# Optimization experiments

Hardware: AMD Instinct MI355X
Metric: run time of the kernel (lower is better)

Reference implementation:

```python
import jax, jax.numpy as jnp
import numpy as np

N_NODES = 50000
N_EDGES = 800000
IN_CH, HID_CH, OUT_CH = 128, 256, 128
BN_EPS = 1e-5


def gcn_conv(x, W, b, src, dst):
    """PyG GCNConv: h = x @ W; symmetric normalization with self-loops; scatter-add; + bias."""
    N = x.shape[0]
    h = x @ W  # [N, out_ch]
    # degree including self-loop (all edge weights = 1)
    deg = jax.ops.segment_sum(jnp.ones(src.shape[0], h.dtype), dst, num_segments=N) + 1.0
    dis = jax.lax.rsqrt(deg)  # deg^-1/2
    norm = dis[src] * dis[dst]  # [E]
    agg = jax.ops.segment_sum(h[src] * norm[:, None], dst, num_segments=N)
    # self-loop contribution: norm_ii = dis[i]^2
    return agg + h * (dis * dis)[:, None] + b


def batchnorm_train(x, gamma, beta):
    mu = jnp.mean(x, axis=0)
    var = jnp.mean((x - mu) ** 2, axis=0)  # biased var, as torch BN uses for normalization
    return (x - mu) * jax.lax.rsqrt(var + BN_EPS) * gamma + beta


def setup_inputs() -> dict:
    key = jax.random.key(0)
    ks = jax.random.split(key, 4)
    x = jax.random.normal(ks[0], (N_NODES, IN_CH), dtype=jnp.float32)
    edge_index = jax.random.randint(ks[1], (2, N_EDGES), 0, N_NODES, dtype=jnp.int64 if jax.config.jax_enable_x64 else jnp.int32)
    W1 = jax.random.normal(ks[2], (IN_CH, HID_CH), dtype=jnp.float32) * (1.0 / np.sqrt(IN_CH))
    W2 = jax.random.normal(ks[3], (HID_CH, OUT_CH), dtype=jnp.float32) * (1.0 / np.sqrt(HID_CH))
    return {
        "x": x,
        "edge_index": edge_index,
        "W1": W1,
        "b1": jnp.zeros((HID_CH,), jnp.float32),
        "gamma1": jnp.ones((HID_CH,), jnp.float32),
        "beta1": jnp.zeros((HID_CH,), jnp.float32),
        "W2": W2,
        "b2": jnp.zeros((OUT_CH,), jnp.float32),
    }


def reference(x, edge_index, W1, b1, gamma1, beta1, W2, b2):
    src, dst = edge_index[0], edge_index[1]
    h = gcn_conv(x, W1, b1, src, dst)
    h = jax.nn.relu(batchnorm_train(h, gamma1, beta1))
    # dropout omitted (deterministic eval-style reference)
    return gcn_conv(h, W2, b2, src, dst)
```

## Files before the change

kernel.cpp:

```cpp
#include <hip/hip_runtime.h>

#define N_NODES 50000
#define N_EDGES 800000
#define C_IN 128
#define C_HID 256
#define C_OUT 128
#define BN_EPS 1e-5f

typedef __bf16 v8bf __attribute__((ext_vector_type(8)));
typedef float f32x4 __attribute__((ext_vector_type(4)));

static __device__ __forceinline__ unsigned short f2bf(float f) {
    unsigned int u = __float_as_uint(f);
    u += 0x7fffu + ((u >> 16) & 1u);
    return (unsigned short)(u >> 16);
}
static __device__ __forceinline__ float bf2f(unsigned short h) {
    return __uint_as_float((unsigned int)h << 16);
}
static __device__ __forceinline__ unsigned int pack2(float a, float b) {
    return (unsigned int)f2bf(a) | ((unsigned int)f2bf(b) << 16);
}
static __device__ __forceinline__ float lo2f(unsigned int u) { return __uint_as_float(u << 16); }
static __device__ __forceinline__ float hi2f(unsigned int u) { return __uint_as_float(u & 0xffff0000u); }

#define DEG_BLOCKS ((N_EDGES + 255) / 256)


__global__ __launch_bounds__(256) void k_deg_wtrans(const int* __restrict__ dst, int* __restrict__ deg,
                                                    const float* __restrict__ W1, const float* __restrict__ W2,
                                                    unsigned short* __restrict__ WT1, unsigned short* __restrict__ WT2) {
    int bx = blockIdx.x, t = threadIdx.x;
    if (bx < DEG_BLOCKS) {
        int e = bx * 256 + t;
        if (e < N_EDGES) atomicAdd(&deg[dst[e]], 1);
    } else {
        int i = (bx - DEG_BLOCKS) * 256 + t;
        if (i < C_IN * C_HID) {
            int n = i >> 7, k = i & 127;
            WT1[n * C_IN + k] = f2bf(W1[k * C_HID + n]);
        } else {
            int j = i - C_IN * C_HID;
            int n = j >> 8, k = j & 255;
            WT2[n * C_HID + k] = f2bf(W2[k * C_OUT + n]);
        }
    }
}


__global__ __launch_bounds__(512) void k_scan1(const int* __restrict__ deg, int* __restrict__ rs,
                                               int* __restrict__ partial, float* __restrict__ dis) {
    __shared__ int s[512];
    int t = threadIdx.x;
    int i = blockIdx.x * 512 + t;
    int v = (i < N_NODES) ? deg[i] : 0;
    if (i < N_NODES) dis[i] = rsqrtf((float)v + 1.0f);
    s[t] = v;
    __syncthreads();
    for (int off = 1; off < 512; off <<= 1) {
        int tv = (t >= off) ? s[t - off] : 0;
        __syncthreads();
        s[t] += tv;
        __syncthreads();
    }
    if (i < N_NODES) rs[i + 1] = s[t];
    if (t == 511) partial[blockIdx.x] = s[511];
}

__global__ __launch_bounds__(256) void k_scan23(int* __restrict__ rs, const int* __restrict__ partial,
                                                int* __restrict__ cur, int nb) {
    __shared__ int pre[128];
    __shared__ int wsum[2];
    int t = threadIdx.x;
    int lane = t & 63;
    int pv = 0, v = 0;
    if (t < 128) {
        pv = (t < nb) ? partial[t] : 0;
        v = pv;
#pragma unroll
        for (int off = 1; off < 64; off <<= 1) {
            int u = __shfl_up(v, off);
            if (lane >= off) v += u;
        }
        if (lane == 63) wsum[t >> 6] = v;
    }
    __syncthreads();
    if (t < 128) {
        if (t >= 64) v += wsum[0];
        pre[t] = v - pv;
    }
    __syncthreads();
    int i = blockIdx.x * 256 + t;
    if (i < N_NODES) {
        int vv = rs[i + 1] + pre[i >> 9];
        rs[i + 1] = vv;
        cur[i + 1] = vv;
    }
    if (i == 0) { rs[0] = 0; cur[0] = 0; }
}


#define SCAT_GROUPS 256
#define NODES_PER_SLICE (N_NODES / 8)
#define EDGES_PER_CHUNK ((N_EDGES + SCAT_GROUPS - 1) / SCAT_GROUPS)
#define SCAT_BLOCKS (SCAT_GROUPS * 8)

__global__ __launch_bounds__(256) void k_scatter_xscale(const int* __restrict__ src, const int* __restrict__ dst,
                                                        int* __restrict__ cur, int* __restrict__ eidx,
                                                        const float* __restrict__ x, const float* __restrict__ dis,
                                                        unsigned short* __restrict__ xs) {
    int bx = blockIdx.x, t = threadIdx.x;
    if (bx < SCAT_BLOCKS) {
        int slice = bx & 7;
        int g = bx >> 3;
        int lo = slice * NODES_PER_SLICE;
        int hi = lo + NODES_PER_SLICE;
        int e0 = g * EDGES_PER_CHUNK;
        int e1 = e0 + EDGES_PER_CHUNK;
        if (e1 > N_EDGES) e1 = N_EDGES;
        for (int e = e0 + t; e < e1; e += 256) {
            int d = dst[e];
            if (d >= lo && d < hi) {
                int pos = atomicAdd(&cur[d], 1);
                eidx[pos] = src[e];
            }
        }
    } else {
        int i = (bx - SCAT_BLOCKS) * 256 + t;
        int node = i >> 4;
        if (node < N_NODES) {
            int g8 = (i & 15) * 8;
            float d = dis[node];
            float4 v0 = *(const float4*)&x[(size_t)node * C_IN + g8];
            float4 v1 = *(const float4*)&x[(size_t)node * C_IN + g8 + 4];
            uint4 o = make_uint4(pack2(v0.x * d, v0.y * d), pack2(v0.z * d, v0.w * d),
                                 pack2(v1.x * d, v1.y * d), pack2(v1.z * d, v1.w * d));
            *(uint4*)&xs[(size_t)node * C_IN + g8] = o;
        }
    }
}


template <bool FINAL>
__global__ __launch_bounds__(256) void k_aggr(const unsigned short* __restrict__ g,
                                              const float* __restrict__ dis, const float* __restrict__ bias,
                                              const int* __restrict__ rs, const int* __restrict__ eidx,
                                              unsigned short* __restrict__ outb, float* __restrict__ outf) {
    int wid = (blockIdx.x * 256 + threadIdx.x) >> 6;
    int lane = threadIdx.x & 63;
    if (wid >= N_NODES) return;
    int slot = lane >> 5;
    int cp = lane & 31;
    int s = rs[wid], e = rs[wid + 1];
    float a0 = 0.f, a1 = 0.f, a2 = 0.f, a3 = 0.f;
    float c0 = 0.f, c1 = 0.f, c2 = 0.f, c3 = 0.f;
    int p = s;
    for (; p + 7 < e; p += 8) {
        int i0 = eidx[p + slot];
        int i1 = eidx[p + 2 + slot];
        int i2 = eidx[p + 4 + slot];
        int i3 = eidx[p + 6 + slot];
        ushort4 v0 = *(const ushort4*)&g[(size_t)i0 * 128 + cp * 4];
        ushort4 v1 = *(const ushort4*)&g[(size_t)i1 * 128 + cp * 4];
        ushort4 v2 = *(const ushort4*)&g[(size_t)i2 * 128 + cp * 4];
        ushort4 v3 = *(const ushort4*)&g[(size_t)i3 * 128 + cp * 4];
        a0 += bf2f(v0.x) + bf2f(v1.x); a1 += bf2f(v0.y) + bf2f(v1.y);
        a2 += bf2f(v0.z) + bf2f(v1.z); a3 += bf2f(v0.w) + bf2f(v1.w);
        c0 += bf2f(v2.x) + bf2f(v3.x); c1 += bf2f(v2.y) + bf2f(v3.y);
        c2 += bf2f(v2.z) + bf2f(v3.z); c3 += bf2f(v2.w) + bf2f(v3.w);
    }
    for (; p + 1 < e; p += 2) {
        int i0 = eidx[p + slot];
        ushort4 v0 = *(const ushort4*)&g[(size_t)i0 * 128 + cp * 4];
        a0 += bf2f(v0.x); a1 += bf2f(v0.y); a2 += bf2f(v0.z); a3 += bf2f(v0.w);
    }
    if (p < e && slot == 0) {
        int i0 = eidx[p];
        ushort4 v0 = *(const ushort4*)&g[(size_t)i0 * 128 + cp * 4];
        a0 += bf2f(v0.x); a1 += bf2f(v0.y); a2 += bf2f(v0.z); a3 += bf2f(v0.w);
    }
    a0 += c0; a1 += c1; a2 += c2; a3 += c3;
    a0 += __shfl_xor(a0, 32); a1 += __shfl_xor(a1, 32);
    a2 += __shfl_xor(a2, 32); a3 += __shfl_xor(a3, 32);
    if (slot == 0) {
        ushort4 gi = *(const ushort4*)&g[(size_t)wid * 128 + cp * 4];
        float d = dis[wid];
        if (FINAL) {
            float4 bv = *(const float4*)&bias[cp * 4];
            float4 o = make_float4(fmaf(d, a0 + bf2f(gi.x), bv.x), fmaf(d, a1 + bf2f(gi.y), bv.y),
                                   fmaf(d, a2 + bf2f(gi.z), bv.z), fmaf(d, a3 + bf2f(gi.w), bv.w));
            *(float4*)&outf[(size_t)wid * 128 + cp * 4] = o;
        } else {
            ushort4 z;
            z.x = f2bf(d * (a0 + bf2f(gi.x)));
            z.y = f2bf(d * (a1 + bf2f(gi.y)));
            z.z = f2bf(d * (a2 + bf2f(gi.z)));
            z.w = f2bf(d * (a3 + bf2f(gi.w)));
            *(ushort4*)&outb[(size_t)wid * 128 + cp * 4] = z;
        }
    }
}


#define GBM 128
#define GBK 64
#define LDA 72

template <bool TRANS>
__global__ __launch_bounds__(256) void k_gemm(const unsigned short* __restrict__ Ah,
                                              const unsigned short* __restrict__ BT,
                                              unsigned short* __restrict__ C,
                                              const float* __restrict__ dis, const float* __restrict__ bias,
                                              float* __restrict__ bnsum, float* __restrict__ bnsq,
                                              const float* __restrict__ gamma, const float* __restrict__ beta,
                                              int M, int N, int K) {
    __shared__ unsigned short Alds[GBM * LDA];
    __shared__ unsigned short Blds[GBM * LDA];
    __shared__ float ep_s[GBM];
    __shared__ float tsc_s[256];
    __shared__ float tof_s[256];
    __shared__ float bnS[128];
    __shared__ float bnQ[128];

    int t = threadIdx.x;
    int row0 = blockIdx.x * GBM;
    int col0 = blockIdx.y * GBM;
    int wave = t >> 6, lane = t & 63;
    int wm = wave & 1, wn = wave >> 1;
    int lm = lane & 15, quad = lane >> 4;

    if (TRANS) {
        if (t < GBM) ep_s[t] = (row0 + t < M) ? dis[row0 + t] : 0.f;
        float inv_n = 1.0f / (float)N_NODES;
        float mu = bnsum[t] * inv_n;
        float var = bnsq[t] * inv_n - mu * mu;
        float a = gamma[t] * rsqrtf(var + BN_EPS);
        tsc_s[t] = a;
        tof_s[t] = beta[t] - mu * a;
    } else {
        if (t < GBM) { ep_s[t] = bias[col0 + t]; bnS[t] = 0.f; bnQ[t] = 0.f; }
    }
    __syncthreads();

    int sr = t >> 1;
    int kb = (t & 1) * 32;

    f32x4 acc[4][4] = {};

    for (int kt = 0; kt < K; kt += GBK) {
        uint4 sa[4], sb[4];
        int r = row0 + sr;
#pragma unroll
        for (int j = 0; j < 4; ++j) {
            int k = kt + kb + 8 * j;
            uint4 h = (r < M) ? *(const uint4*)&Ah[(size_t)r * K + k] : make_uint4(0u, 0u, 0u, 0u);
            if (TRANS) {
                float4 s0 = *(const float4*)&tsc_s[k];
                float4 s1 = *(const float4*)&tsc_s[k + 4];
                float4 o0 = *(const float4*)&tof_s[k];
                float4 o1 = *(const float4*)&tof_s[k + 4];
                float f0 = fmaxf(fmaf(lo2f(h.x), s0.x, o0.x), 0.f);
                float f1 = fmaxf(fmaf(hi2f(h.x), s0.y, o0.y), 0.f);
                float f2 = fmaxf(fmaf(lo2f(h.y), s0.z, o0.z), 0.f);
                float f3 = fmaxf(fmaf(hi2f(h.y), s0.w, o0.w), 0.f);
                float f4 = fmaxf(fmaf(lo2f(h.z), s1.x, o1.x), 0.f);
                float f5 = fmaxf(fmaf(hi2f(h.z), s1.y, o1.y), 0.f);
                float f6 = fmaxf(fmaf(lo2f(h.w), s1.z, o1.z), 0.f);
                float f7 = fmaxf(fmaf(hi2f(h.w), s1.w, o1.w), 0.f);
                sa[j] = make_uint4(pack2(f0, f1), pack2(f2, f3), pack2(f4, f5), pack2(f6, f7));
            } else {
                sa[j] = h;
            }
            sb[j] = *(const uint4*)&BT[(size_t)(col0 + sr) * K + k];
        }
        __syncthreads();
#pragma unroll
        for (int j = 0; j < 4; ++j) {
            *(uint4*)&Alds[sr * LDA + kb + 8 * j] = sa[j];
            *(uint4*)&Blds[sr * LDA + kb + 8 * j] = sb[j];
        }
        __syncthreads();
#pragma unroll
        for (int kc = 0; kc < 2; ++kc) {
            v8bf af[4], bfv[4];
#pragma unroll
            for (int im = 0; im < 4; ++im)
                af[im] = *(const v8bf*)&Alds[(wm * 64 + im * 16 + lm) * LDA + kc * 32 + quad * 8];
#pragma unroll
            for (int in = 0; in < 4; ++in)
                bfv[in] = *(const v8bf*)&Blds[(wn * 64 + in * 16 + lm) * LDA + kc * 32 + quad * 8];
#pragma unroll
            for (int im = 0; im < 4; ++im)
#pragma unroll
                for (int in = 0; in < 4; ++in)
                    acc[im][in] = __builtin_amdgcn_mfma_f32_16x16x32_bf16(af[im], bfv[in], acc[im][in], 0, 0, 0);
        }
    }

    float bs[4] = {0.f, 0.f, 0.f, 0.f}, bq[4] = {0.f, 0.f, 0.f, 0.f};
#pragma unroll
    for (int im = 0; im < 4; ++im) {
        int rb = wm * 64 + im * 16 + quad * 4;
#pragma unroll
        for (int in = 0; in < 4; ++in) {
            f32x4 c = acc[im][in];
            int colLoc = wn * 64 + in * 16 + lm;
            int col = col0 + colLoc;
#pragma unroll
            for (int q = 0; q < 4; ++q) {
                int row = row0 + rb + q;
                if (row < M) {
                    if (TRANS) {
                        C[(size_t)row * N + col] = f2bf(c[q] * ep_s[rb + q]);
                    } else {
                        unsigned short hb = f2bf(c[q] + ep_s[colLoc]);
                        C[(size_t)row * N + col] = hb;
                        float v = bf2f(hb);
                        bs[in] += v;
                        bq[in] = fmaf(v, v, bq[in]);
                    }
                }
            }
        }
    }
    if (!TRANS) {
#pragma unroll
        for (int in = 0; in < 4; ++in) {
            float s = bs[in], q2 = bq[in];
            s += __shfl_xor(s, 16); q2 += __shfl_xor(q2, 16);
            s += __shfl_xor(s, 32); q2 += __shfl_xor(q2, 32);
            if (quad == 0) {
                atomicAdd(&bnS[wn * 64 + in * 16 + lm], s);
                atomicAdd(&bnQ[wn * 64 + in * 16 + lm], q2);
            }
        }
        __syncthreads();
        if (t < 128) {
            atomicAdd(&bnsum[col0 + t], bnS[t]);
            atomicAdd(&bnsq[col0 + t], bnQ[t]);
        }
    }
}


extern "C" void kernel_launch(void* const* d_in, const int* in_sizes, int n_in,
                              void* d_out, int out_size, void* d_ws, size_t ws_size,
                              hipStream_t stream) {
    const float* x      = (const float*)d_in[0];
    const int*   ei     = (const int*)d_in[1];
    const float* W1     = (const float*)d_in[2];
    const float* b1     = (const float*)d_in[3];
    const float* gamma1 = (const float*)d_in[4];
    const float* beta1  = (const float*)d_in[5];
    const float* W2     = (const float*)d_in[6];
    const float* b2     = (const float*)d_in[7];
    const int* srcv = ei;
    const int* dstv = ei + N_EDGES;
    float* out = (float*)d_out;

    char* w = (char*)d_ws;
    size_t off = 0;
    auto alloc = [&](size_t bytes) {
        void* p = w + off;
        off = (off + bytes + 255) & ~(size_t)255;
        return p;
    };
    int*   deg     = (int*)alloc(N_NODES * 4);
    float* bnsum   = (float*)alloc(256 * 4);
    float* bnsq    = (float*)alloc(256 * 4);
    size_t zero_bytes = off;
    float* dis     = (float*)alloc(N_NODES * 4);
    int*   rs      = (int*)alloc((N_NODES + 1) * 4);
    int*   cur     = (int*)alloc((N_NODES + 1) * 4);
    int*   partial = (int*)alloc(128 * 4);
    int*   eidx    = (int*)alloc((size_t)N_EDGES * 4);
    unsigned short* WT1 = (unsigned short*)alloc((size_t)C_IN * C_HID * 2);
    unsigned short* WT2 = (unsigned short*)alloc((size_t)C_HID * C_OUT * 2);
    unsigned short* xs  = (unsigned short*)alloc((size_t)N_NODES * C_IN * 2);
    unsigned short* P   = (unsigned short*)alloc((size_t)N_NODES * C_IN * 2);
    unsigned short* z1  = (unsigned short*)alloc((size_t)N_NODES * C_HID * 2);
    unsigned short* g2  = (unsigned short*)alloc((size_t)N_NODES * C_OUT * 2);
    (void)ws_size; (void)in_sizes; (void)n_in; (void)out_size;

    hipMemsetAsync(deg, 0, zero_bytes, stream);

    int nb = (N_NODES + 511) / 512;
    k_deg_wtrans<<<DEG_BLOCKS + 256, 256, 0, stream>>>(dstv, deg, W1, W2, WT1, WT2);
    k_scan1<<<nb, 512, 0, stream>>>(deg, rs, partial, dis);
    k_scan23<<<(N_NODES + 255) / 256, 256, 0, stream>>>(rs, partial, cur, nb);
    k_scatter_xscale<<<SCAT_BLOCKS + (N_NODES * 16 + 255) / 256, 256, 0, stream>>>(
        srcv, dstv, cur, eidx, x, dis, xs);

    k_aggr<false><<<(N_NODES * 64 + 255) / 256, 256, 0, stream>>>(xs, dis, nullptr, rs, eidx, P, nullptr);
    dim3 gg1((N_NODES + GBM - 1) / GBM, C_HID / GBM);
    k_gemm<false><<<gg1, 256, 0, stream>>>(P, WT1, z1, nullptr, b1, bnsum, bnsq, nullptr, nullptr,
                                           N_NODES, C_HID, C_IN);

    dim3 gg2((N_NODES + GBM - 1) / GBM, C_OUT / GBM);
    k_gemm<true><<<gg2, 256, 0, stream>>>(z1, WT2, g2, dis, nullptr, bnsum, bnsq, gamma1, beta1,
                                          N_NODES, C_OUT, C_HID);
    k_aggr<true><<<(N_NODES * 64 + 255) / 256, 256, 0, stream>>>(g2, dis, b2, rs, eidx, nullptr, out);
}
```

Measured before the change: 300.1 us.

## Rewrite GEMMs to keep weight tile in registers and stream A strips directly

```diff
diff --git a/kernel.cpp b/kernel.cpp
--- a/kernel.cpp
+++ b/kernel.cpp
@@ -202,63 +202,80 @@
 }
 
 
-#define GBM 128
-#define GBK 64
-#define LDA 72
-
-template <bool TRANS>
-__global__ __launch_bounds__(256) void k_gemm(const unsigned short* __restrict__ Ah,
-                                              const unsigned short* __restrict__ BT,
-                                              unsigned short* __restrict__ C,
-                                              const float* __restrict__ dis, const float* __restrict__ bias,
-                                              float* __restrict__ bnsum, float* __restrict__ bnsq,
-                                              const float* __restrict__ gamma, const float* __restrict__ beta,
-                                              int M, int N, int K) {
-    __shared__ unsigned short Alds[GBM * LDA];
-    __shared__ unsigned short Blds[GBM * LDA];
-    __shared__ float ep_s[GBM];
-    __shared__ float tsc_s[256];
-    __shared__ float tof_s[256];
-    __shared__ float bnS[128];
-    __shared__ float bnQ[128];
+template <bool TRANS, int KC>
+__global__ __launch_bounds__(256, 2) void k_gemmv(const unsigned short* __restrict__ Ah,
+                                                  const unsigned short* __restrict__ BT,
+                                                  unsigned short* __restrict__ C,
+                                                  const float* __restrict__ dis, const float* __restrict__ bias,
+                                                  float* __restrict__ bnsum, float* __restrict__ bnsq,
+                                                  const float* __restrict__ gamma, const float* __restrict__ beta,
+                                                  int M, int N) {
+    constexpr int K = KC * 32;
+    constexpr int BP = K + 8;
+    __shared__ unsigned short Blds[64 * BP];
+    __shared__ float tsc_s[K];
+    __shared__ float tof_s[K];
 
     int t = threadIdx.x;
-    int row0 = blockIdx.x * GBM;
-    int col0 = blockIdx.y * GBM;
-    int wave = t >> 6, lane = t & 63;
-    int wm = wave & 1, wn = wave >> 1;
+    int w = t >> 6, lane = t & 63;
     int lm = lane & 15, quad = lane >> 4;
-
-    if (TRANS) {
-        if (t < GBM) ep_s[t] = (row0 + t < M) ? dis[row0 + t] : 0.f;
+    int col0 = blockIdx.y * 64;
+
+    if (TRANS && t < K) {
         float inv_n = 1.0f / (float)N_NODES;
         float mu = bnsum[t] * inv_n;
         float var = bnsq[t] * inv_n - mu * mu;
         float a = gamma[t] * rsqrtf(var + BN_EPS);
         tsc_s[t] = a;
         tof_s[t] = beta[t] - mu * a;
-    } else {
-        if (t < GBM) { ep_s[t] = bias[col0 + t]; bnS[t] = 0.f; bnQ[t] = 0.f; }
-    }
-    __syncthreads();
-
-    int sr = t >> 1;
-    int kb = (t & 1) * 32;
-
-    f32x4 acc[4][4] = {};
-
-    for (int kt = 0; kt < K; kt += GBK) {
-        uint4 sa[4], sb[4];
-        int r = row0 + sr;
-#pragma unroll
-        for (int j = 0; j < 4; ++j) {
-            int k = kt + kb + 8 * j;
-            uint4 h = (r < M) ? *(const uint4*)&Ah[(size_t)r * K + k] : make_uint4(0u, 0u, 0u, 0u);
+    }
+    constexpr int NLD = 64 * K / 8;
+    for (int j = t; j < NLD; j += 256) {
+        int n = j / (K / 8);
+        int kq = j % (K / 8);
+        *(uint4*)&Blds[n * BP + kq * 8] = *(const uint4*)&BT[(size_t)(col0 + n) * K + kq * 8];
+    }
+    __syncthreads();
+    v8bf bfr[4][KC];
+#pragma unroll
+    for (int in = 0; in < 4; ++in)
+#pragma unroll
+        for (int kc = 0; kc < KC; ++kc)
+            bfr[in][kc] = *(const v8bf*)&Blds[(in * 16 + lm) * BP + kc * 32 + quad * 8];
+    __syncthreads();
+
+    unsigned short* Ct = Blds + w * (16 * 80);
+
+    float bias_r[4];
+    if (!TRANS) {
+#pragma unroll
+        for (int in = 0; in < 4; ++in) bias_r[in] = bias[col0 + in * 16 + lm];
+    }
+    float ss[4] = {0.f, 0.f, 0.f, 0.f}, qq[4] = {0.f, 0.f, 0.f, 0.f};
+
+    int strip0 = (blockIdx.x * 4 + w) * 4;
+#pragma unroll
+    for (int s = 0; s < 4; ++s) {
+        int strip = strip0 + s;
+        if (strip * 16 >= M) break;
+        int arow = strip * 16 + lm;
+        uint4 araw[KC];
+#pragma unroll
+        for (int kc = 0; kc < KC; ++kc)
+            araw[kc] = *(const uint4*)&Ah[(size_t)arow * K + kc * 32 + quad * 8];
+        float dqa[4];
+        if (TRANS) *(float4*)dqa = *(const float4*)&dis[strip * 16 + quad * 4];
+        f32x4 acc[4] = {};
+#pragma unroll
+        for (int kc = 0; kc < KC; ++kc) {
+            v8bf af;
             if (TRANS) {
-                float4 s0 = *(const float4*)&tsc_s[k];
-                float4 s1 = *(const float4*)&tsc_s[k + 4];
-                float4 o0 = *(const float4*)&tof_s[k];
-                float4 o1 = *(const float4*)&tof_s[k + 4];
+                int kb2 = kc * 32 + quad * 8;
+                float4 s0 = *(const float4*)&tsc_s[kb2];
+                float4 s1 = *(const float4*)&tsc_s[kb2 + 4];
+                float4 o0 = *(const float4*)&tof_s[kb2];
+                float4 o1 = *(const float4*)&tof_s[kb2 + 4];
+                uint4 h = araw[kc];
                 float f0 = fmaxf(fmaf(lo2f(h.x), s0.x, o0.x), 0.f);
                 float f1 = fmaxf(fmaf(hi2f(h.x), s0.y, o0.y), 0.f);
                 float f2 = fmaxf(fmaf(lo2f(h.y), s0.z, o0.z), 0.f);
@@ -267,77 +284,46 @@
                 float f5 = fmaxf(fmaf(hi2f(h.z), s1.y, o1.y), 0.f);
                 float f6 = fmaxf(fmaf(lo2f(h.w), s1.z, o1.z), 0.f);
                 float f7 = fmaxf(fmaf(hi2f(h.w), s1.w, o1.w), 0.f);
-                sa[j] = make_uint4(pack2(f0, f1), pack2(f2, f3), pack2(f4, f5), pack2(f6, f7));
+                uint4 pk = make_uint4(pack2(f0, f1), pack2(f2, f3), pack2(f4, f5), pack2(f6, f7));
+                af = *(v8bf*)&pk;
             } else {
-                sa[j] = h;
+                af = *(v8bf*)&araw[kc];
             }
-            sb[j] = *(const uint4*)&BT[(size_t)(col0 + sr) * K + k];
-        }
-        __syncthreads();
-#pragma unroll
-        for (int j = 0; j < 4; ++j) {
-            *(uint4*)&Alds[sr * LDA + kb + 8 * j] = sa[j];
-            *(uint4*)&Blds[sr * LDA + kb + 8 * j] = sb[j];
-        }
-        __syncthreads();
-#pragma unroll
-        for (int kc = 0; kc < 2; ++kc) {
-            v8bf af[4], bfv[4];
-#pragma unroll
-            for (int im = 0; im < 4; ++im)
-                af[im] = *(const v8bf*)&Alds[(wm * 64 + im * 16 + lm) * LDA + kc * 32 + quad * 8];
 #pragma unroll
             for (int in = 0; in < 4; ++in)
-                bfv[in] = *(const v8bf*)&Blds[(wn * 64 + in * 16 + lm) * LDA + kc * 32 + quad * 8];
-#pragma unroll
-            for (int im = 0; im < 4; ++im)
-#pragma unroll
-                for (int in = 0; in < 4; ++in)
-                    acc[im][in] = __builtin_amdgcn_mfma_f32_16x16x32_bf16(af[im], bfv[in], acc[im][in], 0, 0, 0);
-        }
-    }
-
-    float bs[4] = {0.f, 0.f, 0.f, 0.f}, bq[4] = {0.f, 0.f, 0.f, 0.f};
-#pragma unroll
-    for (int im = 0; im < 4; ++im) {
-        int rb = wm * 64 + im * 16 + quad * 4;
+                acc[in] = __builtin_amdgcn_mfma_f32_16x16x32_bf16(af, bfr[in][kc], acc[in], 0, 0, 0);
+        }
 #pragma unroll
         for (int in = 0; in < 4; ++in) {
-            f32x4 c = acc[im][in];
-            int colLoc = wn * 64 + in * 16 + lm;
-            int col = col0 + colLoc;
 #pragma unroll
             for (int q = 0; q < 4; ++q) {
-                int row = row0 + rb + q;
-                if (row < M) {
-                    if (TRANS) {
-                        C[(size_t)row * N + col] = f2bf(c[q] * ep_s[rb + q]);
-                    } else {
-                        unsigned short hb = f2bf(c[q] + ep_s[colLoc]);
-                        C[(size_t)row * N + col] = hb;
-                        float v = bf2f(hb);
-                        bs[in] += v;
-                        bq[in] = fmaf(v, v, bq[in]);
-                    }
+                float val = TRANS ? acc[in][q] * dqa[q] : acc[in][q] + bias_r[in];
+                unsigned short hb = f2bf(val);
+                Ct[(quad * 4 + q) * 80 + in * 16 + lm] = hb;
+                if (!TRANS) {
+                    float v = bf2f(hb);
+                    ss[in] += v;
+                    qq[in] = fmaf(v, v, qq[in]);
                 }
             }
         }
+#pragma unroll
+        for (int it = 0; it < 2; ++it) {
+            int rl = (lane >> 3) + it * 8;
+            uint4 v = *(const uint4*)&Ct[rl * 80 + (lane & 7) * 8];
+            *(uint4*)&C[(size_t)(strip * 16 + rl) * N + col0 + (lane & 7) * 8] = v;
+        }
     }
     if (!TRANS) {
 #pragma unroll
         for (int in = 0; in < 4; ++in) {
-            float s = bs[in], q2 = bq[in];
+            float s = ss[in], q2 = qq[in];
             s += __shfl_xor(s, 16); q2 += __shfl_xor(q2, 16);
             s += __shfl_xor(s, 32); q2 += __shfl_xor(q2, 32);
             if (quad == 0) {
-                atomicAdd(&bnS[wn * 64 + in * 16 + lm], s);
-                atomicAdd(&bnQ[wn * 64 + in * 16 + lm], q2);
+                atomicAdd(&bnsum[col0 + in * 16 + lm], s);
+                atomicAdd(&bnsq[col0 + in * 16 + lm], q2);
             }
-        }
-        __syncthreads();
-        if (t < 128) {
-            atomicAdd(&bnsum[col0 + t], bnS[t]);
-            atomicAdd(&bnsq[col0 + t], bnQ[t]);
         }
     }
 }
@@ -392,12 +378,12 @@
         srcv, dstv, cur, eidx, x, dis, xs);
 
     k_aggr<false><<<(N_NODES * 64 + 255) / 256, 256, 0, stream>>>(xs, dis, nullptr, rs, eidx, P, nullptr);
-    dim3 gg1((N_NODES + GBM - 1) / GBM, C_HID / GBM);
-    k_gemm<false><<<gg1, 256, 0, stream>>>(P, WT1, z1, nullptr, b1, bnsum, bnsq, nullptr, nullptr,
-                                           N_NODES, C_HID, C_IN);
-
-    dim3 gg2((N_NODES + GBM - 1) / GBM, C_OUT / GBM);
-    k_gemm<true><<<gg2, 256, 0, stream>>>(z1, WT2, g2, dis, nullptr, bnsum, bnsq, gamma1, beta1,
-                                          N_NODES, C_OUT, C_HID);
+    dim3 gg1((N_NODES + 255) / 256, C_HID / 64);
+    k_gemmv<false, 4><<<gg1, 256, 0, stream>>>(P, WT1, z1, nullptr, b1, bnsum, bnsq, nullptr, nullptr,
+                                               N_NODES, C_HID);
+
+    dim3 gg2((N_NODES + 255) / 256, C_OUT / 64);
+    k_gemmv<true, 8><<<gg2, 256, 0, stream>>>(z1, WT2, g2, dis, nullptr, bnsum, bnsq, gamma1, beta1,
+                                              N_NODES, C_OUT);
     k_aggr<true><<<(N_NODES * 64 + 255) / 256, 256, 0, stream>>>(g2, dis, b2, rs, eidx, nullptr, out);
 }
```

Measured after the change: 287.2 us. 4.3% less time.
